# Kernel optimization log

Measured on AMD Instinct MI355X. Metric: run time of the kernel, lower is better.

Reference implementation:

```python
import jax, jax.numpy as jnp
import numpy as np

N_NODES = 10000
N_EDGES = 160000
C = 16        # num_feature_channels
C2 = 8        # output channels per irrep per head (C/2)
HID = 64      # radial_network_hidden_units
NH = 2        # num_attention_heads
NG = 16       # graphs in batch
F_IN = 64     # num_features
F_OUT = 32    # number_of_output_features
HEAD_TYPES = ("normal", "inverse")  # invariant_dictionary
IRREP_SLICES = ((0, 1), (1, 4), (4, 9))  # l=0,1,2 blocks of the SH dim


def _sph_harm(r):
    """Component-normalized real spherical harmonics l=0..2 for unit vectors r [E,3] -> [E,9]."""
    x, y, z = r[:, 0], r[:, 1], r[:, 2]
    c3 = 1.7320508   # sqrt(3)
    c15 = 3.8729833  # sqrt(15)
    l0 = jnp.ones_like(x)[:, None]
    l1 = c3 * r
    l2 = jnp.stack([
        c15 * x * y,
        c15 * y * z,
        1.1180340 * (2.0 * z * z - x * x - y * y),  # sqrt(5)/2
        c15 * x * z,
        1.9364917 * (x * x - y * y),                 # sqrt(15)/2
    ], axis=-1)
    return jnp.concatenate([l0, l1, l2], axis=-1)


def setup_inputs() -> dict:
    key = jax.random.key(0)
    ks = jax.random.split(key, 16)
    node_features = jax.random.normal(ks[0], (N_NODES, F_IN), jnp.float32)
    pos = jax.random.normal(ks[1], (N_NODES, 3), jnp.float32)
    src = jax.random.randint(ks[2], (N_EDGES,), 0, N_NODES)
    off = jax.random.randint(ks[3], (N_EDGES,), 1, N_NODES)  # avoid self-loops (d=0)
    tgt = (src + off) % N_NODES
    edge_index = jnp.stack([src, tgt], axis=0)
    batch = jnp.sort(jax.random.randint(ks[4], (N_NODES,), 0, NG))
    s = lambda k, shape, fan: (jax.random.normal(k, shape, jnp.float32) / np.sqrt(fan)).astype(jnp.float32)
    return dict(
        node_features=node_features, pos=pos,
        W_embed=s(ks[5], (F_IN, C), F_IN), b_embed=jnp.zeros((C,), jnp.float32),
        Wq=s(ks[6], (NH, C, C), C), Wk=s(ks[7], (NH, C, C), C),
        W1=s(ks[8], (NH, 1, HID), 1), b1=jnp.zeros((NH, HID), jnp.float32),
        Wa=s(ks[9], (NH, HID), HID), Wv=s(ks[10], (NH, HID, C * 3), HID),
        Wo=s(ks[11], (NH, 3, C, C2), C),
        Wproj=s(ks[12], (NH * C2, F_OUT), NH * C2), bproj=jnp.zeros((F_OUT,), jnp.float32),
        edge_index=edge_index, batch=batch,
    )


def _forward(node_features, pos, W_embed, b_embed, Wq, Wk, W1, b1, Wa, Wv, Wo,
             Wproj, bproj, edge_index, batch):
    src, tgt = edge_index[0], edge_index[1]
    rel = pos[tgt] - pos[src]                       # [E,3]
    dist = jnp.linalg.norm(rel, axis=-1, keepdims=True)  # [E,1]
    rhat = rel / dist
    Y = _sph_harm(rhat)                             # [E,9]
    x = node_features @ W_embed + b_embed          # [N,C] scalar (0e) features
    xs = x[src]                                     # [E,C]
    inv_sqrt_c = 1.0 / np.sqrt(C)
    head_outs = []
    for h in range(NH):
        d_feat = dist if HEAD_TYPES[h] == "normal" else dist ** -2  # [E,1]
        hid = jax.nn.relu(d_feat @ W1[h] + b1[h])   # [E,HID] radial network
        att_bias = hid @ Wa[h]                      # [E]
        wv = (hid @ Wv[h]).reshape(-1, C, 3)        # [E,C,3] per-(channel,l) radial weights
        q = x @ Wq[h]
        k = x @ Wk[h]
        logit = jnp.sum(q[tgt] * k[src], axis=-1) * inv_sqrt_c + att_bias  # [E]
        # segment softmax over incoming edges of each target node
        m = jax.ops.segment_max(logit, tgt, num_segments=N_NODES)
        e = jnp.exp(logit - m[tgt])
        z = jax.ops.segment_sum(e, tgt, num_segments=N_NODES)
        alpha = e / z[tgt]                          # [E]
        # expand per-l weights to per-m: dims (1,3,5)
        wv_m = jnp.repeat(wv, np.array([1, 3, 5]), axis=2, total_repeat_length=9)  # [E,C,9]
        msg = (alpha[:, None, None] * wv_m) * xs[:, :, None] * Y[:, None, :]       # [E,C,9]
        node_out = jax.ops.segment_sum(msg, tgt, num_segments=N_NODES)             # [N,C,9]
        parts = [jnp.einsum('ncm,co->nom', node_out[:, :, s0:s1], Wo[h, li]).reshape(N_NODES, -1)
                 for li, (s0, s1) in enumerate(IRREP_SLICES)]
        head_outs.append(jnp.concatenate(parts, axis=-1))  # [N, C2*9]
    feat = jnp.concatenate(head_outs, axis=-1)              # [N, NH*C2*9]
    pooled = jax.ops.segment_sum(feat, batch, num_segments=NG)  # [NG, NH*C2*9]
    # equivariant Linear -> F_OUT x 0e: only scalar (l=0) components map to scalars
    blk = C2 * 9
    scal = jnp.concatenate([pooled[:, h * blk: h * blk + C2] for h in range(NH)], axis=-1)  # [NG, NH*C2]
    return scal @ Wproj + bproj                             # [NG, F_OUT]


def reference(node_features, pos, W_embed, b_embed, Wq, Wk, W1, b1, Wa, Wv, Wo,
              Wproj, bproj, edge_index, batch):
    return _forward(node_features, pos, W_embed, b_embed, Wq, Wk, W1, b1, Wa, Wv,
                    Wo, Wproj, bproj, edge_index, batch)
```

## Files before the change

kernel.cpp:

```cpp
#include <hip/hip_runtime.h>
#include <math.h>

#define NN 10000
#define NE 160000
#define CAP 96

__device__ __forceinline__ unsigned bf16pack2(float a, float b) {
    unsigned ua = __float_as_uint(a);
    unsigned ub = __float_as_uint(b);
    ua = ua + 0x7fffu + ((ua >> 16) & 1u);
    ub = ub + 0x7fffu + ((ub >> 16) & 1u);
    return (ua >> 16) | (ub & 0xffff0000u);
}

__global__ __launch_bounds__(256) void k_xqk(const float* __restrict__ nf,
        const float* __restrict__ We, const float* __restrict__ be,
        const float* __restrict__ Wq, const float* __restrict__ Wk,
        const float* __restrict__ Wv,
        float* __restrict__ x, float* __restrict__ q, float* __restrict__ k,
        int* __restrict__ zeroReg, float* __restrict__ vC) {
    int t = threadIdx.x;
    int gid = blockIdx.x * 256 + t;
    if (gid < 10256) zeroReg[gid] = 0;
    if (blockIdx.x == 0) {
        for (int i = t; i < 2048; i += 256) {
            int h = i >> 10, j = (i >> 4) & 63, c = i & 15;
            vC[i] = Wv[(h * 64 + j) * 48 + 3 * c];
        }
    }
    __shared__ float sWe[64 * 16];
    __shared__ float sWq[2 * 16 * 16];
    __shared__ float sWk[2 * 16 * 16];
    __shared__ float sNF[16 * 64];
    __shared__ float sX[16 * 16];
    for (int i = t; i < 1024; i += 256) sWe[i] = We[i];
    for (int i = t; i < 512; i += 256) { sWq[i] = Wq[i]; sWk[i] = Wk[i]; }
    int nodeBase = blockIdx.x * 16;
    for (int i = t; i < 1024; i += 256) {
        int n = nodeBase + (i >> 6);
        sNF[i] = (n < NN) ? nf[n * 64 + (i & 63)] : 0.0f;
    }
    __syncthreads();
    int ln = t >> 4, c = t & 15;
    int n = nodeBase + ln;
    float acc = be[c];
    #pragma unroll 16
    for (int j = 0; j < 64; ++j) acc = fmaf(sNF[ln * 64 + j], sWe[j * 16 + c], acc);
    sX[ln * 16 + c] = acc;
    __syncthreads();
    if (n < NN) {
        x[n * 16 + c] = acc;
        #pragma unroll
        for (int h = 0; h < 2; ++h) {
            float aq = 0.0f, ak = 0.0f;
            #pragma unroll
            for (int j = 0; j < 16; ++j) {
                float xv = sX[ln * 16 + j];
                aq = fmaf(xv, sWq[(h * 16 + j) * 16 + c], aq);
                ak = fmaf(xv, sWk[(h * 16 + j) * 16 + c], ak);
            }
            q[(n * 2 + h) * 16 + c] = aq;
            k[(n * 2 + h) * 16 + c] = ak;
        }
    }
}

__global__ __launch_bounds__(256) void k_edge(const float* __restrict__ pos,
        const int* __restrict__ ei,
        const float* __restrict__ q, const float* __restrict__ k,
        const float* __restrict__ W1, const float* __restrict__ b1,
        const float* __restrict__ Wa, const float* __restrict__ vC,
        const float* __restrict__ Wo,
        const float* __restrict__ x, int* __restrict__ deg,
        float* __restrict__ lgp, uint4* __restrict__ gb) {
    int e = blockIdx.x * 256 + threadIdx.x;
    if (e >= NE) return;
    int s = ei[e], t = ei[NE + e];
    int p = atomicAdd(&deg[t], 1);
    bool ok = (p < CAP);
    size_t slot = (size_t)t * CAP + p;
    float dx = pos[t * 3 + 0] - pos[s * 3 + 0];
    float dy = pos[t * 3 + 1] - pos[s * 3 + 1];
    float dz = pos[t * 3 + 2] - pos[s * 3 + 2];
    float d = sqrtf(dx * dx + dy * dy + dz * dz);
    float fh[2] = { d, 1.0f / (d * d) };
    const float4* xp = (const float4*)(x + (size_t)s * 16);
    float4 xs0 = xp[0], xs1 = xp[1], xs2 = xp[2], xs3 = xp[3];
    float xf[16] = { xs0.x, xs0.y, xs0.z, xs0.w, xs1.x, xs1.y, xs1.z, xs1.w,
                     xs2.x, xs2.y, xs2.z, xs2.w, xs3.x, xs3.y, xs3.z, xs3.w };
    float L2v[2];
    #pragma unroll
    for (int h = 0; h < 2; ++h) {
        const float4* qt = (const float4*)(q + (size_t)t * 32 + h * 16);
        const float4* ks = (const float4*)(k + (size_t)s * 32 + h * 16);
        float4 a0 = qt[0], a1 = qt[1], a2 = qt[2], a3 = qt[3];
        float4 b0 = ks[0], c1 = ks[1], c2 = ks[2], c3 = ks[3];
        float dot = a0.x * b0.x + a0.y * b0.y + a0.z * b0.z + a0.w * b0.w
                  + a1.x * c1.x + a1.y * c1.y + a1.z * c1.z + a1.w * c1.w
                  + a2.x * c2.x + a2.y * c2.y + a2.z * c2.z + a2.w * c2.w
                  + a3.x * c3.x + a3.y * c3.y + a3.z * c3.z + a3.w * c3.w;
        float f = fh[h];
        float att = 0.0f;
        float acc[16];
        #pragma unroll
        for (int c = 0; c < 16; ++c) acc[c] = 0.0f;
        const float* w1b = W1 + h * 64;
        const float* b1b = b1 + h * 64;
        const float* wab = Wa + h * 64;
        const float* vcb = vC + h * 1024;
        #pragma unroll 8
        for (int j = 0; j < 64; ++j) {
            float hid = fmaxf(fmaf(f, w1b[j], b1b[j]), 0.0f);
            att = fmaf(hid, wab[j], att);
            #pragma unroll
            for (int c = 0; c < 16; ++c)
                acc[c] = fmaf(hid, vcb[j * 16 + c], acc[c]);
        }
        L2v[h] = fmaf(dot, 0.25f, att);
        float g[8];
        #pragma unroll
        for (int o = 0; o < 8; ++o) g[o] = 0.0f;
        const float* wob = Wo + h * 384;
        #pragma unroll
        for (int c = 0; c < 16; ++c) {
            float axc = acc[c] * xf[c];
            #pragma unroll
            for (int o = 0; o < 8; ++o) g[o] = fmaf(axc, wob[c * 8 + o], g[o]);
        }
        if (ok) {
            gb[slot * 2 + h] = make_uint4(bf16pack2(g[0], g[1]), bf16pack2(g[2], g[3]),
                                          bf16pack2(g[4], g[5]), bf16pack2(g[6], g[7]));
        }
    }
    if (ok) *(float2*)(lgp + slot * 2) = make_float2(L2v[0], L2v[1]);
}

__global__ __launch_bounds__(256) void k_gather(const int* __restrict__ deg,
        const float* __restrict__ lgp, const unsigned* __restrict__ gb,
        float* __restrict__ feat) {
    int t0 = threadIdx.x;
    int wv = t0 >> 6;
    int lane = t0 & 63;
    int pid = blockIdx.x * 4 + wv;
    int n = pid >> 1, h = pid & 1;
    int dg = min(deg[n], CAP);
    int g = lane >> 2, p = lane & 3;
    float m = -INFINITY, z = 0.0f, u0 = 0.0f, u1 = 0.0f;
    const float* lgb = lgp + (size_t)n * (CAP * 2) + h;
    const unsigned* gbb = gb + (size_t)n * (CAP * 8) + h * 4 + p;
    for (int i = g; i < dg; i += 16) {
        float L = lgb[i * 2];
        unsigned wbits = gbb[(size_t)i * 8];
        float ga = __uint_as_float(wbits << 16);
        float gbv = __uint_as_float(wbits & 0xffff0000u);
        float nm = fmaxf(m, L);
        float sc = (m > -INFINITY) ? __expf(m - nm) : 0.0f;
        float w  = __expf(L - nm);
        u0 = fmaf(u0, sc, w * ga);
        u1 = fmaf(u1, sc, w * gbv);
        z  = fmaf(z, sc, w);
        m = nm;
    }
    #pragma unroll
    for (int off = 4; off <= 32; off <<= 1) {
        float mo = __shfl_xor(m, off, 64);
        float zo = __shfl_xor(z, off, 64);
        float a0o = __shfl_xor(u0, off, 64);
        float a1o = __shfl_xor(u1, off, 64);
        float nm = fmaxf(m, mo);
        float a = (m  > -INFINITY) ? __expf(m  - nm) : 0.0f;
        float b = (mo > -INFINITY) ? __expf(mo - nm) : 0.0f;
        u0 = u0 * a + a0o * b;
        u1 = u1 * a + a1o * b;
        z  = z * a + zo * b;
        m = nm;
    }
    if (lane < 4) {
        float inv = (z > 0.0f) ? 1.0f / z : 0.0f;
        *(float2*)(feat + n * 16 + h * 8 + p * 2) = make_float2(u0 * inv, u1 * inv);
    }
}

__global__ __launch_bounds__(256) void k_pool(const float* __restrict__ feat,
        const int* __restrict__ batch, float* __restrict__ pooled) {
    __shared__ float sP[256];
    int t = threadIdx.x;
    sP[t] = 0.0f;
    __syncthreads();
    int tid = blockIdx.x * 256 + t;
    int c = tid & 15, seg = tid >> 4;
    int n0 = seg * 16, n1 = min(n0 + 16, NN);
    float run = 0.0f;
    int curg = -1;
    for (int n = n0; n < n1; ++n) {
        int gg = batch[n];
        if (gg != curg) {
            if (curg >= 0) atomicAdd(&sP[curg * 16 + c], run);
            run = 0.0f; curg = gg;
        }
        run += feat[n * 16 + c];
    }
    if (curg >= 0) atomicAdd(&sP[curg * 16 + c], run);
    __syncthreads();
    atomicAdd(&pooled[t], sP[t]);
}

__global__ __launch_bounds__(512) void k_final(const float* __restrict__ pooled,
        const float* __restrict__ Wproj, const float* __restrict__ bproj,
        float* __restrict__ out) {
    int t = threadIdx.x;
    int g = t >> 5, fo = t & 31;
    float acc = bproj[fo];
    #pragma unroll
    for (int j = 0; j < 16; ++j) acc = fmaf(pooled[g * 16 + j], Wproj[j * 32 + fo], acc);
    out[g * 32 + fo] = acc;
}

extern "C" void kernel_launch(void* const* d_in, const int* in_sizes, int n_in,
                              void* d_out, int out_size, void* d_ws, size_t ws_size,
                              hipStream_t stream) {
    const float* nf    = (const float*)d_in[0];
    const float* pos   = (const float*)d_in[1];
    const float* We    = (const float*)d_in[2];
    const float* be    = (const float*)d_in[3];
    const float* Wq    = (const float*)d_in[4];
    const float* Wk    = (const float*)d_in[5];
    const float* W1    = (const float*)d_in[6];
    const float* b1    = (const float*)d_in[7];
    const float* Wa    = (const float*)d_in[8];
    const float* Wv    = (const float*)d_in[9];
    const float* Wo    = (const float*)d_in[10];
    const float* Wproj = (const float*)d_in[11];
    const float* bproj = (const float*)d_in[12];
    const int*   ei    = (const int*)d_in[13];
    const int*   batch = (const int*)d_in[14];
    float* out = (float*)d_out;
    (void)in_sizes; (void)n_in; (void)out_size; (void)ws_size;

    float* ws     = (float*)d_ws;
    float* x      = ws;
    float* q      = x + 160000;
    float* k      = q + 320000;
    float* feat   = k + 320000;
    float* pooled = feat + 160000;
    int*   deg    = (int*)(pooled + 256);
    float* vC     = (float*)(deg + 10000);
    float* lgp    = vC + 2048;
    unsigned* gbu = (unsigned*)(lgp + (size_t)NN * CAP * 2);

    hipLaunchKernelGGL(k_xqk,    dim3(625),  dim3(256), 0, stream, nf, We, be, Wq, Wk, Wv, x, q, k, (int*)pooled, vC);
    hipLaunchKernelGGL(k_edge,   dim3(625),  dim3(256), 0, stream, pos, ei, q, k, W1, b1, Wa, vC, Wo, x, deg, lgp, (uint4*)gbu);
    hipLaunchKernelGGL(k_gather, dim3(5000), dim3(256), 0, stream, deg, lgp, gbu, feat);
    hipLaunchKernelGGL(k_pool,   dim3(40),   dim3(256), 0, stream, feat, batch, pooled);
    hipLaunchKernelGGL(k_final,  dim3(1),    dim3(512), 0, stream, pooled, Wproj, bproj, out);
}
```

Baseline: 130.7 us.

## Replace per-edge radial MLP with piecewise-linear breakpoint table lookup

Since the radial network is a one-input ReLU MLP followed by linear maps, its outputs are piecewise linear in the scalar feature. Block 0 of the first kernel sorts the 64 ReLU breakpoints per head and builds prefix-summed slope and intercept tables for the attention logit and the 16 value channels. The edge kernel loads this table into shared memory, binary-searches the segment for each edge and evaluates one fma per channel, replacing the 64x17 FMA loop. This adds serial table construction in one block of the first kernel and a shared-memory load per edge block, and changes floating-point summation order.

```diff
diff --git a/kernel.cpp b/kernel.cpp
--- a/kernel.cpp
+++ b/kernel.cpp
@@ -4,6 +4,12 @@
 #define NN 10000
 #define NE 160000
 #define CAP 96
+#define TPH 2432
+#define AATT_OFF 64
+#define BATT_OFF 132
+#define A_OFF 200
+#define B_OFF 1312
+
 
 __device__ __forceinline__ unsigned bf16pack2(float a, float b) {
     unsigned ua = __float_as_uint(a);
@@ -16,23 +22,21 @@
 __global__ __launch_bounds__(256) void k_xqk(const float* __restrict__ nf,
         const float* __restrict__ We, const float* __restrict__ be,
         const float* __restrict__ Wq, const float* __restrict__ Wk,
-        const float* __restrict__ Wv,
+        const float* __restrict__ W1, const float* __restrict__ b1,
+        const float* __restrict__ Wa, const float* __restrict__ Wv,
         float* __restrict__ x, float* __restrict__ q, float* __restrict__ k,
-        int* __restrict__ zeroReg, float* __restrict__ vC) {
+        int* __restrict__ zeroReg, float* __restrict__ tab) {
     int t = threadIdx.x;
     int gid = blockIdx.x * 256 + t;
     if (gid < 10256) zeroReg[gid] = 0;
-    if (blockIdx.x == 0) {
-        for (int i = t; i < 2048; i += 256) {
-            int h = i >> 10, j = (i >> 4) & 63, c = i & 15;
-            vC[i] = Wv[(h * 64 + j) * 48 + 3 * c];
-        }
-    }
     __shared__ float sWe[64 * 16];
     __shared__ float sWq[2 * 16 * 16];
     __shared__ float sWk[2 * 16 * 16];
     __shared__ float sNF[16 * 64];
     __shared__ float sX[16 * 16];
+    __shared__ float sT[2][64], sDA[2][64], sDB[2][64], sIA[2][64], sIB[2][64];
+    __shared__ float sW[2][64][17];
+    __shared__ short sOrd[2][64];
     for (int i = t; i < 1024; i += 256) sWe[i] = We[i];
     for (int i = t; i < 512; i += 256) { sWq[i] = Wq[i]; sWk[i] = Wk[i]; }
     int nodeBase = blockIdx.x * 16;
@@ -63,17 +67,71 @@
             k[(n * 2 + h) * 16 + c] = ak;
         }
     }
+    if (blockIdx.x == 0) {
+        if (t < 128) {
+            int h = t >> 6, j = t & 63;
+            float a = W1[h * 64 + j], b = b1[h * 64 + j];
+            float da = 0.0f, db = 0.0f, ia = 0.0f, ib = 0.0f, th;
+            if (a > 0.0f)      { th = -b / a; da = a;  db = b; }
+            else if (a < 0.0f) { th = -b / a; da = -a; db = -b; ia = a; ib = b; }
+            else               { th = INFINITY; if (b > 0.0f) ib = b; }
+            sT[h][j] = th; sDA[h][j] = da; sDB[h][j] = db; sIA[h][j] = ia; sIB[h][j] = ib;
+        }
+        for (int i = t; i < 2 * 64 * 17; i += 256) {
+            int h = i / 1088, r = i % 1088, j = r / 17, cc = r % 17;
+            sW[h][j][cc] = (cc < 16) ? Wv[(h * 64 + j) * 48 + 3 * cc] : Wa[h * 64 + j];
+        }
+        __syncthreads();
+        if (t < 128) {
+            int h = t >> 6, j = t & 63;
+            float tj = sT[h][j];
+            int r = 0;
+            #pragma unroll 16
+            for (int kk = 0; kk < 64; ++kk) {
+                float tk = sT[h][kk];
+                r += (tk < tj || (tk == tj && kk < j)) ? 1 : 0;
+            }
+            sOrd[h][r] = (short)j;
+            tab[h * TPH + r] = tj;
+        }
+        __syncthreads();
+        if (t < 34) {
+            int h = t / 17, cc = t % 17;
+            float A = 0.0f, B = 0.0f;
+            #pragma unroll 8
+            for (int j = 0; j < 64; ++j) {
+                float w = sW[h][j][cc];
+                A = fmaf(sIA[h][j], w, A);
+                B = fmaf(sIB[h][j], w, B);
+            }
+            float* pa; float* pb; int stride;
+            if (cc == 16) { pa = tab + h * TPH + AATT_OFF; pb = tab + h * TPH + BATT_OFF; stride = 1; }
+            else          { pa = tab + h * TPH + A_OFF + cc; pb = tab + h * TPH + B_OFF + cc; stride = 17; }
+            pa[0] = A; pb[0] = B;
+            #pragma unroll 8
+            for (int sg = 1; sg <= 64; ++sg) {
+                int u = sOrd[h][sg - 1];
+                float w = sW[h][u][cc];
+                A = fmaf(sDA[h][u], w, A);
+                B = fmaf(sDB[h][u], w, B);
+                pa[sg * stride] = A;
+                pb[sg * stride] = B;
+            }
+        }
+    }
 }
 
 __global__ __launch_bounds__(256) void k_edge(const float* __restrict__ pos,
         const int* __restrict__ ei,
         const float* __restrict__ q, const float* __restrict__ k,
-        const float* __restrict__ W1, const float* __restrict__ b1,
-        const float* __restrict__ Wa, const float* __restrict__ vC,
-        const float* __restrict__ Wo,
-        const float* __restrict__ x, int* __restrict__ deg,
+        const float* __restrict__ Wo, const float* __restrict__ x,
+        const float* __restrict__ tab, int* __restrict__ deg,
         float* __restrict__ lgp, uint4* __restrict__ gb) {
-    int e = blockIdx.x * 256 + threadIdx.x;
+    __shared__ float sTab[2 * TPH];
+    int tid = threadIdx.x;
+    for (int i = tid; i < 2 * TPH; i += 256) sTab[i] = tab[i];
+    __syncthreads();
+    int e = blockIdx.x * 256 + tid;
     if (e >= NE) return;
     int s = ei[e], t = ei[NE + e];
     int p = atomicAdd(&deg[t], 1);
@@ -83,7 +141,7 @@
     float dy = pos[t * 3 + 1] - pos[s * 3 + 1];
     float dz = pos[t * 3 + 2] - pos[s * 3 + 2];
     float d = sqrtf(dx * dx + dy * dy + dz * dz);
-    float fh[2] = { d, 1.0f / (d * d) };
+    float fh2[2] = { d, 1.0f / (d * d) };
     const float4* xp = (const float4*)(x + (size_t)s * 16);
     float4 xs0 = xp[0], xs1 = xp[1], xs2 = xp[2], xs3 = xp[3];
     float xf[16] = { xs0.x, xs0.y, xs0.z, xs0.w, xs1.x, xs1.y, xs1.z, xs1.w,
@@ -99,31 +157,24 @@
                   + a1.x * c1.x + a1.y * c1.y + a1.z * c1.z + a1.w * c1.w
                   + a2.x * c2.x + a2.y * c2.y + a2.z * c2.z + a2.w * c2.w
                   + a3.x * c3.x + a3.y * c3.y + a3.z * c3.z + a3.w * c3.w;
-        float f = fh[h];
-        float att = 0.0f;
-        float acc[16];
+        float f = fh2[h];
+        const float* tb = sTab + h * TPH;
+        int sg = 0;
         #pragma unroll
-        for (int c = 0; c < 16; ++c) acc[c] = 0.0f;
-        const float* w1b = W1 + h * 64;
-        const float* b1b = b1 + h * 64;
-        const float* wab = Wa + h * 64;
-        const float* vcb = vC + h * 1024;
-        #pragma unroll 8
-        for (int j = 0; j < 64; ++j) {
-            float hid = fmaxf(fmaf(f, w1b[j], b1b[j]), 0.0f);
-            att = fmaf(hid, wab[j], att);
-            #pragma unroll
-            for (int c = 0; c < 16; ++c)
-                acc[c] = fmaf(hid, vcb[j * 16 + c], acc[c]);
-        }
+        for (int st = 32; st >= 1; st >>= 1)
+            if (tb[sg + st - 1] < f) sg += st;
+        if (tb[sg] < f) ++sg;
+        float att = fmaf(tb[AATT_OFF + sg], f, tb[BATT_OFF + sg]);
         L2v[h] = fmaf(dot, 0.25f, att);
+        const float* Ab = tb + A_OFF + sg * 17;
+        const float* Bb = tb + B_OFF + sg * 17;
+        const float* wob = Wo + h * 384;
         float g[8];
         #pragma unroll
         for (int o = 0; o < 8; ++o) g[o] = 0.0f;
-        const float* wob = Wo + h * 384;
         #pragma unroll
         for (int c = 0; c < 16; ++c) {
-            float axc = acc[c] * xf[c];
+            float axc = fmaf(Ab[c], f, Bb[c]) * xf[c];
             #pragma unroll
             for (int o = 0; o < 8; ++o) g[o] = fmaf(axc, wob[c * 8 + o], g[o]);
         }
@@ -244,12 +295,12 @@
     float* feat   = k + 320000;
     float* pooled = feat + 160000;
     int*   deg    = (int*)(pooled + 256);
-    float* vC     = (float*)(deg + 10000);
-    float* lgp    = vC + 2048;
+    float* tab    = (float*)(deg + 10000);
+    float* lgp    = tab + 4864;
     unsigned* gbu = (unsigned*)(lgp + (size_t)NN * CAP * 2);
 
-    hipLaunchKernelGGL(k_xqk,    dim3(625),  dim3(256), 0, stream, nf, We, be, Wq, Wk, Wv, x, q, k, (int*)pooled, vC);
-    hipLaunchKernelGGL(k_edge,   dim3(625),  dim3(256), 0, stream, pos, ei, q, k, W1, b1, Wa, vC, Wo, x, deg, lgp, (uint4*)gbu);
+    hipLaunchKernelGGL(k_xqk,    dim3(625),  dim3(256), 0, stream, nf, We, be, Wq, Wk, W1, b1, Wa, Wv, x, q, k, (int*)pooled, tab);
+    hipLaunchKernelGGL(k_edge,   dim3(625),  dim3(256), 0, stream, pos, ei, q, k, Wo, x, tab, deg, lgp, (uint4*)gbu);
     hipLaunchKernelGGL(k_gather, dim3(5000), dim3(256), 0, stream, deg, lgp, gbu, feat);
     hipLaunchKernelGGL(k_pool,   dim3(40),   dim3(256), 0, stream, feat, batch, pooled);
     hipLaunchKernelGGL(k_final,  dim3(1),    dim3(512), 0, stream, pooled, Wproj, bproj, out);
```

Measured after the change: 138.9 us. +6.3%, slower.
